# Optimization experiments

Measured on AMD Instinct MI355X. Metric: run time of the kernel, lower is better.

Reference implementation:

```python
import jax, jax.numpy as jnp
import numpy as np

B, S, D, H, L, V, DFF = 8, 1024, 256, 8, 4, 100, 1024
EPS = 1e-5


def _pos_encodings(seq_len, d):
    # Faithful to SinusoidalPositionalEmbedding (NOTE: original uses sin for both halves)
    pos = jnp.arange(seq_len, dtype=jnp.float32)[:, None]        # [S,1]
    freqs = jnp.arange(d, dtype=jnp.float32)[None, :]            # [1,D]
    sin_even = jnp.sin(pos / 10000.0 ** (freqs[:, 0::2] / d))    # [S,D/2]
    sin_odd = jnp.sin(pos / 10000.0 ** (freqs[:, 1::2] / d))     # [S,D/2]
    return jnp.concatenate([sin_even, sin_odd], axis=1)          # [S,D]


def _self_attention_mask(sequence_length, seq_len):
    # create_self_attention_mask with causal=True; assumes max(sequence_length)==seq_len
    r = jnp.arange(seq_len)[None, :]                             # [1,S]
    m = (r < sequence_length[:, None]).astype(jnp.float32)       # [B,S]
    m = m[:, :, None] * m[:, None, :]                            # [B,S,S]
    causal = jnp.tril(jnp.ones((seq_len, seq_len), jnp.float32))
    return m * causal                                            # [B,S,S]


def setup_inputs() -> dict:
    key = jax.random.key(0)
    ks = jax.random.split(key, 20)
    n = lambda k, shape, s=0.02: (jax.random.normal(k, shape) * s).astype(jnp.float32)
    return {
        "output_ids": jax.random.randint(ks[0], (B, S), 0, V),
        "target_sequence_length": jnp.full((B,), S, dtype=jnp.int32),
        "embedding": n(ks[1], (V, D), 1.0),
        "Wq": n(ks[2], (L, D, D)), "bq": jnp.zeros((L, D), jnp.float32),
        "Wk": n(ks[3], (L, D, D)), "bk": jnp.zeros((L, D), jnp.float32),
        "Wv": n(ks[4], (L, D, D)), "bv": jnp.zeros((L, D), jnp.float32),
        "Wo": n(ks[5], (L, D, D)), "bo": jnp.zeros((L, D), jnp.float32),
        "W1": n(ks[6], (L, D, DFF)), "b1": jnp.zeros((L, DFF), jnp.float32),
        "W2": n(ks[7], (L, DFF, D)), "b2": jnp.zeros((L, D), jnp.float32),
        "g1": jnp.ones((L, D), jnp.float32), "be1": jnp.zeros((L, D), jnp.float32),
        "g2": jnp.ones((L, D), jnp.float32), "be2": jnp.zeros((L, D), jnp.float32),
        "Wc": n(ks[8], (D, V)), "bc": jnp.zeros((V,), jnp.float32),
    }


def _forward(output_ids, target_sequence_length, embedding, Wq, bq, Wk, bk, Wv, bv,
             Wo, bo, W1, b1, W2, b2, g1, be1, g2, be2, Wc, bc):
    Bn, Sn = output_ids.shape
    d = embedding.shape[1]
    x = embedding[output_ids] + _pos_encodings(Sn, d)[None]      # [B,S,D]
    mask = _self_attention_mask(target_sequence_length, Sn)[:, None] > 0  # [B,1,S,S] bool

    def ln(h, g, b):
        m = h.mean(-1, keepdims=True)
        v = jnp.var(h, axis=-1, keepdims=True)
        return (h - m) / jnp.sqrt(v + EPS) * g + b

    def step(x, p):
        wq, bq_, wk, bk_, wv, bv_, wo, bo_, w1, b1_, w2, b2_, g1_, be1_, g2_, be2_ = p
        q = (x @ wq + bq_).reshape(Bn, Sn, H, -1)
        k = (x @ wk + bk_).reshape(Bn, Sn, H, -1)
        v = (x @ wv + bv_).reshape(Bn, Sn, H, -1)
        dh = q.shape[-1]
        scores = jnp.einsum('bqhd,bkhd->bhqk', q, k) / jnp.sqrt(jnp.float32(dh))
        attn = jax.nn.softmax(jnp.where(mask, scores, -1e9), axis=-1)
        attn = jnp.where(mask, attn, 0.0)                        # post-softmax mask (as original)
        y = jnp.einsum('bhqk,bkhd->bqhd', attn, v).reshape(Bn, Sn, -1)
        y = y @ wo + bo_
        x = ln(x + y, g1_, be1_)
        ff = jax.nn.relu(x @ w1 + b1_) @ w2 + b2_
        x = ln(x + ff, g2_, be2_)
        return x, None

    x, _ = jax.lax.scan(step, x, (Wq, bq, Wk, bk, Wv, bv, Wo, bo, W1, b1, W2, b2, g1, be1, g2, be2))
    return x @ Wc + bc                                           # logits [B,S,V]


def reference(output_ids, target_sequence_length, embedding, Wq, bq, Wk, bk, Wv, bv,
              Wo, bo, W1, b1, W2, b2, g1, be1, g2, be2, Wc, bc):
    return _forward(output_ids, target_sequence_length, embedding, Wq, bq, Wk, bk, Wv, bv,
                    Wo, bo, W1, b1, W2, b2, g1, be1, g2, be2, Wc, bc)
```

## Files before the change

### kernel.cpp

```cpp
#include <hip/hip_runtime.h>
#include <hip/hip_bf16.h>
#include <stdint.h>

#define B_   8
#define S_   1024
#define D_   256
#define H_   8
#define DH_  32
#define L_   4
#define V_   100
#define DFF_ 1024
#define M_   (B_*S_)

using bf16 = __hip_bfloat16;
typedef __bf16 bf16x8 __attribute__((ext_vector_type(8)));
typedef float  f32x4  __attribute__((ext_vector_type(4)));

static __device__ __forceinline__ float b2f(unsigned short u) {
  union { unsigned int i; float f; } w; w.i = ((unsigned int)u) << 16; return w.f;
}
static __device__ __forceinline__ unsigned short f2b(float f) {
  bf16 h = (bf16)f; return *(unsigned short*)&h;
}

static __device__ __forceinline__ void load_lds16(const void* g, void* l) {
  __builtin_amdgcn_global_load_lds((const __attribute__((address_space(1))) void*)g,
                                   (__attribute__((address_space(3))) void*)l,
                                   16, 0, 0);
}

#define SRC_CHS(tid)  ((((tid) & 3) ^ (((tid) >> 3) & 3)) * 8)
#define FRAG_Q8(quad, l15)  (((quad) ^ (((l15) >> 1) & 3)) * 8)

template<int CTRL>
static __device__ __forceinline__ float dppf(float v) {
  union { float f; int i; } a, r;
  a.f = v;
  r.i = __builtin_amdgcn_update_dpp(0, a.i, CTRL, 0xF, 0xF, true);
  return r.f;
}
static __device__ __forceinline__ float red_sum16(float v) {
  v += dppf<0xB1>(v);
  v += dppf<0x4E>(v);
  v += dppf<0x141>(v);
  v += dppf<0x140>(v);
  return v;
}

__global__ void prep_t(const float* __restrict__ Wq, const float* __restrict__ Wk,
                       const float* __restrict__ Wv, const float* __restrict__ Wo,
                       const float* __restrict__ W1, const float* __restrict__ W2,
                       const float* __restrict__ Wc,
                       const float* __restrict__ bq, const float* __restrict__ bk,
                       const float* __restrict__ bv,
                       bf16* __restrict__ WqkvT, bf16* __restrict__ WoT,
                       bf16* __restrict__ W1T, bf16* __restrict__ W2T,
                       bf16* __restrict__ WcT, float* __restrict__ bqkv)
{
  const int z = blockIdx.z;
  if (z == 25) {
    if (blockIdx.x || blockIdx.y) return;
    const int tid = threadIdx.y*32 + threadIdx.x;
    for (int i = tid; i < L_*768; i += 256) {
      const int l2 = i / 768, j = i % 768;
      const float* src = (j < 256) ? bq : (j < 512) ? bk : bv;
      bqkv[i] = src[l2*256 + (j & 255)];
    }
    return;
  }
  const float* src; bf16* dst; int R, C, Cd;
  if (z < 12) {
    const int l = z / 3, w = z % 3;
    src = ((w == 0) ? Wq : (w == 1) ? Wk : Wv) + (size_t)l*65536;
    R = 256; C = 256; Cd = 256;
    dst = WqkvT + (size_t)l*196608 + (size_t)w*65536;
  } else if (z < 16) {
    const int l = z - 12;
    src = Wo + (size_t)l*65536; R = 256; C = 256; Cd = 256;
    dst = WoT + (size_t)l*65536;
  } else if (z < 20) {
    const int l = z - 16;
    src = W1 + (size_t)l*262144; R = 256; C = 1024; Cd = 1024;
    dst = W1T + (size_t)l*262144;
  } else if (z < 24) {
    const int l = z - 20;
    src = W2 + (size_t)l*262144; R = 1024; C = 256; Cd = 256;
    dst = W2T + (size_t)l*262144;
  } else {
    src = Wc; R = 256; C = 100; Cd = 128;
    dst = WcT;
  }
  const int c0 = blockIdx.x*32, r0 = blockIdx.y*32;
  if (c0 >= Cd || r0 >= R) return;
  __shared__ float t[32][33];
  #pragma unroll
  for (int i = 0; i < 4; ++i) {
    const int r = r0 + threadIdx.y + i*8;
    const int c = c0 + threadIdx.x;
    t[threadIdx.y + i*8][threadIdx.x] = (r < R && c < C) ? src[(size_t)r*C + c] : 0.f;
  }
  __syncthreads();
  #pragma unroll
  for (int i = 0; i < 4; ++i) {
    const int c = c0 + threadIdx.y + i*8;
    const int r = r0 + threadIdx.x;
    if (c < Cd && r < R)
      dst[(size_t)c*R + r] = (bf16)t[threadIdx.x][threadIdx.y + i*8];
  }
}

__global__ void embed_kernel(const int* __restrict__ ids, const float* __restrict__ emb,
                             bf16* __restrict__ x)
{
  const int bs = blockIdx.x;
  const int d  = threadIdx.x;
  const int s  = bs & (S_-1);
  const int id = ids[bs];
  const int f  = (d < 128) ? (2*d) : (2*(d-128)+1);
  const float inv = powf(10000.f, -(float)f * (1.f/256.f));
  const float pe  = sinf((float)s * inv);
  x[(size_t)bs*D_ + d] = (bf16)(emb[(size_t)id*D_ + d] + pe);
}

__global__ __launch_bounds__(256) void gemm_qkv(
    const bf16* __restrict__ A, const bf16* __restrict__ BT,
    const float* __restrict__ bias,
    bf16* __restrict__ qp, bf16* __restrict__ kp, bf16* __restrict__ vt)
{
  __shared__ bf16 As[128*32];
  __shared__ bf16 Bs[64*32];
  __shared__ bf16 Vs[64][136];
  const int tid  = threadIdx.x;
  const int lane = tid & 63, wave = tid >> 6;
  const int quad = lane >> 4, l15 = lane & 15;
  const int m0 = blockIdx.x * 128;
  const int n0 = blockIdx.y * 64;
  const int wm = (wave & 1) * 64;
  const int wn = (wave >> 1) * 32;
  const int K = 256;

  const bf16* a0 = A  + (size_t)m0 * K;
  const bf16* b0 = BT + (size_t)n0 * K;
  const int row = tid >> 2;
  const int chs = SRC_CHS(tid);
  const int q8  = FRAG_Q8(quad, l15);

  f32x4 acc[4][2] = {};

  for (int k0 = 0; k0 < K; k0 += 32) {
    __syncthreads();
    load_lds16(a0 + (size_t)row*K      + k0 + chs, (char*)As + (size_t)wave*1024);
    load_lds16(a0 + (size_t)(row+64)*K + k0 + chs, (char*)As + 4096 + (size_t)wave*1024);
    load_lds16(b0 + (size_t)row*K      + k0 + chs, (char*)Bs + (size_t)wave*1024);
    __syncthreads();
    bf16x8 af[4], bfr[2];
    #pragma unroll
    for (int mt = 0; mt < 4; ++mt)
      af[mt] = *(const bf16x8*)(As + (wm + mt*16 + l15)*32 + q8);
    #pragma unroll
    for (int nt = 0; nt < 2; ++nt)
      bfr[nt] = *(const bf16x8*)(Bs + (wn + nt*16 + l15)*32 + q8);
    #pragma unroll
    for (int mt = 0; mt < 4; ++mt)
      #pragma unroll
      for (int nt = 0; nt < 2; ++nt)
        acc[mt][nt] = __builtin_amdgcn_mfma_f32_16x16x32_bf16(af[mt], bfr[nt], acc[mt][nt], 0, 0, 0);
  }

  const int seg = n0 >> 8;
  const int b  = m0 >> 10;
  const int s0 = m0 & 1023;

  if (seg < 2) {
    bf16* dst = seg ? kp : qp;
    const float sc = seg ? 1.f : (0.17677669529663687f * 1.4426950408889634f);
    #pragma unroll
    for (int nt = 0; nt < 2; ++nt) {
      const int n  = n0 + wn + nt*16 + l15;
      const int nn = n & 255;
      const int h = nn >> 5, d = nn & 31;
      const float bvs = bias[n];
      bf16* hb = dst + (((size_t)b*H_ + h)*S_)*DH_ + d;
      #pragma unroll
      for (int mt = 0; mt < 4; ++mt) {
        const int ml = wm + mt*16 + quad*4;
        #pragma unroll
        for (int r = 0; r < 4; ++r)
          hb[(size_t)(s0 + ml + r)*DH_] = (bf16)((acc[mt][nt][r] + bvs) * sc);
      }
    }
  } else {
    #pragma unroll
    for (int nt = 0; nt < 2; ++nt) {
      const int nl = wn + nt*16 + l15;
      const float bvs = bias[n0 + nl];
      #pragma unroll
      for (int mt = 0; mt < 4; ++mt) {
        const int ml = wm + mt*16 + quad*4;
        #pragma unroll
        for (int r = 0; r < 4; ++r)
          Vs[nl][ml + r] = (bf16)(acc[mt][nt][r] + bvs);
      }
    }
    __syncthreads();
    #pragma unroll
    for (int t = 0; t < 2; ++t) {
      const int vrow = (tid >> 3) + 32*t;
      const int soff = (tid & 7) * 16;
      const int nn = (n0 + vrow) & 255;
      const int h = nn >> 5, d = nn & 31;
      bf16* dst = vt + (((size_t)b*H_ + h)*DH_ + d)*S_ + s0 + soff;
      *(bf16x8*)dst       = *(const bf16x8*)&Vs[vrow][soff];
      *(bf16x8*)(dst + 8) = *(const bf16x8*)&Vs[vrow][soff + 8];
    }
  }
}

template<bool RELU, bool OUT_BF16>
__global__ __launch_bounds__(256) void gemm_bt(
    const bf16* __restrict__ A, const bf16* __restrict__ BT,
    const float* __restrict__ bias, void* __restrict__ C,
    int M, int N, int K)
{
  __shared__ bf16 As[128*32];
  __shared__ bf16 Bs[64*32];
  const int tid  = threadIdx.x;
  const int lane = tid & 63, wave = tid >> 6;
  const int quad = lane >> 4, l15 = lane & 15;
  const int m0 = blockIdx.x * 128;
  const int n0 = blockIdx.y * 64;
  const int wm = (wave & 1) * 64;
  const int wn = (wave >> 1) * 32;

  const bf16* a0 = A  + (size_t)m0 * K;
  const bf16* b0 = BT + (size_t)n0 * K;
  const int row = tid >> 2;
  const int chs = SRC_CHS(tid);
  const int q8  = FRAG_Q8(quad, l15);

  f32x4 acc[4][2] = {};

  for (int k0 = 0; k0 < K; k0 += 32) {
    __syncthreads();
    load_lds16(a0 + (size_t)row*K      + k0 + chs, (char*)As + (size_t)wave*1024);
    load_lds16(a0 + (size_t)(row+64)*K + k0 + chs, (char*)As + 4096 + (size_t)wave*1024);
    load_lds16(b0 + (size_t)row*K      + k0 + chs, (char*)Bs + (size_t)wave*1024);
    __syncthreads();
    bf16x8 af[4], bfr[2];
    #pragma unroll
    for (int mt = 0; mt < 4; ++mt)
      af[mt] = *(const bf16x8*)(As + (wm + mt*16 + l15)*32 + q8);
    #pragma unroll
    for (int nt = 0; nt < 2; ++nt)
      bfr[nt] = *(const bf16x8*)(Bs + (wn + nt*16 + l15)*32 + q8);
    #pragma unroll
    for (int mt = 0; mt < 4; ++mt)
      #pragma unroll
      for (int nt = 0; nt < 2; ++nt)
        acc[mt][nt] = __builtin_amdgcn_mfma_f32_16x16x32_bf16(af[mt], bfr[nt], acc[mt][nt], 0, 0, 0);
  }

  #pragma unroll
  for (int nt = 0; nt < 2; ++nt) {
    const int n = n0 + wn + nt*16 + l15;
    const float bvs = bias[n];
    #pragma unroll
    for (int mt = 0; mt < 4; ++mt) {
      const int mr = m0 + wm + mt*16 + quad*4;
      #pragma unroll
      for (int r = 0; r < 4; ++r) {
        float v = acc[mt][nt][r] + bvs;
        if (RELU) v = fmaxf(v, 0.f);
        if (OUT_BF16) ((bf16*)C)[(size_t)(mr + r)*N + n] = (bf16)v;
        else          ((float*)C)[(size_t)(mr + r)*N + n] = v;
      }
    }
  }
}

template<bool RELU, bool OUT_BF16, bool NMASK>
__global__ __launch_bounds__(256) void gemm_bt64(
    const bf16* __restrict__ A, const bf16* __restrict__ BT,
    const float* __restrict__ bias, void* __restrict__ C,
    int M, int N, int K)
{
  __shared__ bf16 As[64*32];
  __shared__ bf16 Bs[64*32];
  const int tid  = threadIdx.x;
  const int lane = tid & 63, wave = tid >> 6;
  const int quad = lane >> 4, l15 = lane & 15;
  const int m0 = blockIdx.x * 64;
  const int n0 = blockIdx.y * 64;
  const int wm = (wave & 1) * 32;
  const int wn = (wave >> 1) * 32;

  const bf16* a0 = A  + (size_t)m0 * K;
  const bf16* b0 = BT + (size_t)n0 * K;
  const int row = tid >> 2;
  const int chs = SRC_CHS(tid);
  const int q8  = FRAG_Q8(quad, l15);

  f32x4 acc[2][2] = {};

  for (int k0 = 0; k0 < K; k0 += 32) {
    __syncthreads();
    load_lds16(a0 + (size_t)row*K + k0 + chs, (char*)As + (size_t)wave*1024);
    load_lds16(b0 + (size_t)row*K + k0 + chs, (char*)Bs + (size_t)wave*1024);
    __syncthreads();
    bf16x8 af[2], bfr[2];
    #pragma unroll
    for (int mt = 0; mt < 2; ++mt)
      af[mt] = *(const bf16x8*)(As + (wm + mt*16 + l15)*32 + q8);
    #pragma unroll
    for (int nt = 0; nt < 2; ++nt)
      bfr[nt] = *(const bf16x8*)(Bs + (wn + nt*16 + l15)*32 + q8);
    #pragma unroll
    for (int mt = 0; mt < 2; ++mt)
      #pragma unroll
      for (int nt = 0; nt < 2; ++nt)
        acc[mt][nt] = __builtin_amdgcn_mfma_f32_16x16x32_bf16(af[mt], bfr[nt], acc[mt][nt], 0, 0, 0);
  }

  #pragma unroll
  for (int nt = 0; nt < 2; ++nt) {
    const int n = n0 + wn + nt*16 + l15;
    if (NMASK && n >= N) continue;
    const float bvs = bias[n];
    #pragma unroll
    for (int mt = 0; mt < 2; ++mt) {
      const int mr = m0 + wm + mt*16 + quad*4;
      #pragma unroll
      for (int r = 0; r < 4; ++r) {
        float v = acc[mt][nt][r] + bvs;
        if (RELU) v = fmaxf(v, 0.f);
        if (OUT_BF16) ((bf16*)C)[(size_t)(mr + r)*N + n] = (bf16)v;
        else          ((float*)C)[(size_t)(mr + r)*N + n] = v;
      }
    }
  }
}

__global__ __launch_bounds__(256) void gemm_ln(
    const bf16* __restrict__ A, const bf16* __restrict__ BT,
    const float* __restrict__ bias, const float* __restrict__ g,
    const float* __restrict__ be, bf16* xio, int K)
{
  __shared__ bf16 As[16*32];
  __shared__ bf16 Bs[256*32];
  __shared__ bf16 Xs[16][264];
  __shared__ float sums[4][16][2];

  const int tid  = threadIdx.x;
  const int lane = tid & 63, wave = tid >> 6;
  const int quad = lane >> 4, l15 = lane & 15;
  const int m0 = blockIdx.x * 16;
  const int wn = wave * 64;

  const bf16* a0 = A + (size_t)m0 * K;
  const int chs = SRC_CHS(tid);
  const int q8  = FRAG_Q8(quad, l15);

  f32x4 acc[4] = {};

  for (int k0 = 0; k0 < K; k0 += 32) {
    __syncthreads();
    if (wave == 0)
      load_lds16(a0 + (size_t)(lane >> 2)*K + k0 + SRC_CHS(lane), (char*)As);
    #pragma unroll
    for (int j = 0; j < 4; ++j)
      load_lds16(BT + (size_t)(64*j + (tid >> 2))*K + k0 + chs,
                 (char*)Bs + j*4096 + (size_t)wave*1024);
    __syncthreads();
    const bf16x8 af = *(const bf16x8*)(As + l15*32 + q8);
    #pragma unroll
    for (int nt = 0; nt < 4; ++nt) {
      const bf16x8 bfr = *(const bf16x8*)(Bs + (wn + nt*16 + l15)*32 + q8);
      acc[nt] = __builtin_amdgcn_mfma_f32_16x16x32_bf16(af, bfr, acc[nt], 0, 0, 0);
    }
  }

  {
    const int xr = tid >> 4, xc = (tid & 15) * 16;
    const bf16* src = xio + (size_t)(m0 + xr)*D_ + xc;
    *(bf16x8*)&Xs[xr][xc]     = *(const bf16x8*)src;
    *(bf16x8*)&Xs[xr][xc + 8] = *(const bf16x8*)(src + 8);
  }
  __syncthreads();

  float v[4][4];
  float bvs[4];
  #pragma unroll
  for (int nt = 0; nt < 4; ++nt) bvs[nt] = bias[wn + nt*16 + l15];
  #pragma unroll
  for (int r = 0; r < 4; ++r) {
    const int rr = quad*4 + r;
    float ls = 0.f, lq = 0.f;
    #pragma unroll
    for (int nt = 0; nt < 4; ++nt) {
      const float y = acc[nt][r] + bvs[nt];
      const float xv = b2f(*(const unsigned short*)&Xs[rr][wn + nt*16 + l15]);
      const float vv = xv + y;
      v[r][nt] = vv;
      ls += vv;
      lq += vv*vv;
    }
    ls = red_sum16(ls);
    lq = red_sum16(lq);
    if (l15 == 0) { sums[wave][rr][0] = ls; sums[wave][rr][1] = lq; }
  }
  __syncthreads();

  float gv[4], bev[4];
  #pragma unroll
  for (int nt = 0; nt < 4; ++nt) {
    gv[nt]  = g[wn + nt*16 + l15];
    bev[nt] = be[wn + nt*16 + l15];
  }
  #pragma unroll
  for (int r = 0; r < 4; ++r) {
    const int rr = quad*4 + r;
    const float ts = sums[0][rr][0] + sums[1][rr][0] + sums[2][rr][0] + sums[3][rr][0];
    const float tq = sums[0][rr][1] + sums[1][rr][1] + sums[2][rr][1] + sums[3][rr][1];
    const float mean = ts * (1.f/256.f);
    const float var  = tq * (1.f/256.f) - mean*mean;
    const float inv  = rsqrtf(var + 1e-5f);
    #pragma unroll
    for (int nt = 0; nt < 4; ++nt) {
      const bf16 o = (bf16)((v[r][nt] - mean)*inv*gv[nt] + bev[nt]);
      Xs[rr][wn + nt*16 + l15] = o;
    }
  }
  __syncthreads();

  {
    const int xr = tid >> 4, xc = (tid & 15) * 16;
    bf16* dst = xio + (size_t)(m0 + xr)*D_ + xc;
    *(bf16x8*)dst       = *(const bf16x8*)&Xs[xr][xc];
    *(bf16x8*)(dst + 8) = *(const bf16x8*)&Xs[xr][xc + 8];
  }
}

#define PSTR 68
__global__ __launch_bounds__(256) void attn_kernel(
    const bf16* __restrict__ qp, const bf16* __restrict__ kp,
    const bf16* __restrict__ vt, const int* __restrict__ tsl,
    bf16* __restrict__ out)
{
  const int h = blockIdx.y, b = blockIdx.z;
  const int lane = threadIdx.x & 63, wave = threadIdx.x >> 6;
  const int quad = lane >> 4, l15 = lane & 15;
  const int sid = blockIdx.x + wave*16;
  const int q0 = sid*16;
  const int len = tsl[b];

  __shared__ bf16 Pl[4][16*PSTR];

  const size_t bh = (size_t)b*H_ + h;
  const bf16* qb = qp + bh*S_*DH_;
  const bf16* kb = kp + bh*S_*DH_;
  const bf16* vb = vt + bh*DH_*S_;

  const bf16x8 qf = *(const bf16x8*)(qb + (size_t)(q0 + l15)*DH_ + quad*8);

  float lacc = 0.f;
  f32x4 o0 = {0.f,0.f,0.f,0.f}, o1 = {0.f,0.f,0.f,0.f};

  bf16* pw = &Pl[wave][0];
  const int qr = q0 + l15;
  const bool full = (len >= S_);
  const int dt = sid >> 2;

  bf16x8 kf[4];
  #pragma unroll
  for (int nt = 0; nt < 4; ++nt)
    kf[nt] = *(const bf16x8*)(kb + (size_t)(nt*16 + l15)*DH_ + quad*8);

  for (int ks = 0; ks <= dt; ++ks) {
    const int k0 = ks*64;
    bf16x8 vf[4];
    #pragma unroll
    for (int kc = 0; kc < 2; ++kc) {
      vf[kc*2]   = *(const bf16x8*)(vb + (size_t)l15*S_      + k0 + kc*32 + quad*8);
      vf[kc*2+1] = *(const bf16x8*)(vb + (size_t)(16+l15)*S_ + k0 + kc*32 + quad*8);
    }
    f32x4 s[4];
    #pragma unroll
    for (int nt = 0; nt < 4; ++nt) {
      const f32x4 z = {0.f,0.f,0.f,0.f};
      s[nt] = __builtin_amdgcn_mfma_f32_16x16x32_bf16(kf[nt], qf, z, 0, 0, 0);
    }
    bf16x8 kn[4];
    if (ks < dt) {
      const int k1 = k0 + 64;
      #pragma unroll
      for (int nt = 0; nt < 4; ++nt)
        kn[nt] = *(const bf16x8*)(kb + (size_t)(k1 + nt*16 + l15)*DH_ + quad*8);
    }
    #pragma unroll
    for (int nt = 0; nt < 4; ++nt) {
      float p0, p1, p2, p3;
      if (full && ks < dt) {
        p0 = exp2f(s[nt][0]);
        p1 = exp2f(s[nt][1]);
        p2 = exp2f(s[nt][2]);
        p3 = exp2f(s[nt][3]);
      } else {
        const int kbase = k0 + nt*16 + quad*4;
        const bool okq = (qr < len);
        p0 = (okq && kbase+0 <= qr && kbase+0 < len) ? exp2f(s[nt][0]) : 0.f;
        p1 = (okq && kbase+1 <= qr && kbase+1 < len) ? exp2f(s[nt][1]) : 0.f;
        p2 = (okq && kbase+2 <= qr && kbase+2 < len) ? exp2f(s[nt][2]) : 0.f;
        p3 = (okq && kbase+3 <= qr && kbase+3 < len) ? exp2f(s[nt][3]) : 0.f;
      }
      lacc += (p0 + p1) + (p2 + p3);
      uint2 w;
      w.x = (unsigned)f2b(p0) | ((unsigned)f2b(p1) << 16);
      w.y = (unsigned)f2b(p2) | ((unsigned)f2b(p3) << 16);
      *(uint2*)((char*)pw + l15*(PSTR*2) + nt*32 + quad*8) = w;
    }
    asm volatile("s_waitcnt lgkmcnt(0)" ::: "memory");
    #pragma unroll
    for (int kc = 0; kc < 2; ++kc) {
      const bf16x8 pf = *(const bf16x8*)(pw + l15*PSTR + kc*32 + quad*8);
      o0 = __builtin_amdgcn_mfma_f32_16x16x32_bf16(pf, vf[kc*2],   o0, 0, 0, 0);
      o1 = __builtin_amdgcn_mfma_f32_16x16x32_bf16(pf, vf[kc*2+1], o1, 0, 0, 0);
    }
    if (ks < dt) {
      #pragma unroll
      for (int nt = 0; nt < 4; ++nt) kf[nt] = kn[nt];
    }
  }

  float lt = lacc;
  lt += __shfl_xor(lt, 16);
  lt += __shfl_xor(lt, 32);

  bf16* ob = out + (size_t)b*S_*D_ + h*DH_;
  #pragma unroll
  for (int r = 0; r < 4; ++r) {
    const float lr = __shfl(lt, (lane & 48) | (quad*4 + r));
    const float inv = 1.f / fmaxf(lr, 1e-30f);
    const size_t rowoff = (size_t)(q0 + quad*4 + r)*D_;
    ob[rowoff + l15]      = (bf16)(o0[r]*inv);
    ob[rowoff + 16 + l15] = (bf16)(o1[r]*inv);
  }
}

extern "C" void kernel_launch(void* const* d_in, const int* in_sizes, int n_in,
                              void* d_out, int out_size, void* d_ws, size_t ws_size,
                              hipStream_t stream)
{
  const int*   ids = (const int*)d_in[0];
  const int*   tsl = (const int*)d_in[1];
  const float* emb = (const float*)d_in[2];
  const float* Wq  = (const float*)d_in[3];
  const float* bq  = (const float*)d_in[4];
  const float* Wk  = (const float*)d_in[5];
  const float* bk  = (const float*)d_in[6];
  const float* Wv  = (const float*)d_in[7];
  const float* bv  = (const float*)d_in[8];
  const float* Wo  = (const float*)d_in[9];
  const float* bo  = (const float*)d_in[10];
  const float* W1  = (const float*)d_in[11];
  const float* b1  = (const float*)d_in[12];
  const float* W2  = (const float*)d_in[13];
  const float* b2  = (const float*)d_in[14];
  const float* g1  = (const float*)d_in[15];
  const float* be1 = (const float*)d_in[16];
  const float* g2  = (const float*)d_in[17];
  const float* be2 = (const float*)d_in[18];
  const float* Wc  = (const float*)d_in[19];
  const float* bc  = (const float*)d_in[20];

  if (ws_size < (size_t)40*1024*1024) return;

  char* p = (char*)d_ws;
  auto carve = [&](size_t bytes) { void* r = (void*)p; p += (bytes + 255) & ~(size_t)255; return r; };
  bf16*  x     = (bf16*) carve((size_t)M_*D_*2);
  char*  big   = (char*) carve((size_t)M_*DFF_*2);
  char*  pkbuf = (char*) carve((size_t)12*1024*1024);
  bf16*  WqkvT = (bf16*) carve((size_t)L_*768*256*2);
  bf16*  WoT   = (bf16*) carve((size_t)L_*65536*2);
  bf16*  W1T   = (bf16*) carve((size_t)L_*262144*2);
  bf16*  W2T   = (bf16*) carve((size_t)L_*262144*2);
  bf16*  WcT   = (bf16*) carve((size_t)128*256*2);
  float* bqkv  = (float*)carve((size_t)L_*768*4);

  bf16*  aout = (bf16*)big;
  bf16*  ff1  = (bf16*)big;
  bf16*  qp   = (bf16*)pkbuf;
  bf16*  kp   = (bf16*)(pkbuf + (size_t)4*1024*1024);
  bf16*  vt   = (bf16*)(pkbuf + (size_t)8*1024*1024);

  prep_t<<<dim3(32,32,26), dim3(32,8), 0, stream>>>(Wq,Wk,Wv,Wo,W1,W2,Wc,bq,bk,bv,
                                                    WqkvT,WoT,W1T,W2T,WcT,bqkv);
  embed_kernel<<<dim3(M_), 256, 0, stream>>>(ids, emb, x);

  for (int l = 0; l < L_; ++l) {
    gemm_qkv<<<dim3(64,12), 256, 0, stream>>>(
        x, WqkvT + (size_t)l*768*256, bqkv + l*768, qp, kp, vt);
    attn_kernel<<<dim3(16,8,8), 256, 0, stream>>>(qp, kp, vt, tsl, aout);
    gemm_ln<<<dim3(512), 256, 0, stream>>>(
        aout, WoT + (size_t)l*65536, bo + l*256, g1 + l*256, be1 + l*256, x, 256);
    gemm_bt<true,true><<<dim3(64,16), 256, 0, stream>>>(
        x, W1T + (size_t)l*262144, b1 + l*1024, ff1, M_, 1024, 256);
    gemm_ln<<<dim3(512), 256, 0, stream>>>(
        ff1, W2T + (size_t)l*262144, b2 + l*256, g2 + l*256, be2 + l*256, x, 1024);
  }

  gemm_bt64<false,false,true><<<dim3(128,2), 256, 0, stream>>>(
      x, WcT, bc, (float*)d_out, M_, V_, 256);
}
```

Measured before the change: 464.1 us.

## Split attention key range across two blocks and combine partials

Each query tile's causal key range is split into two halves handled by separate blocks, doubling grid size, and a new combine kernel sums the unnormalized partial outputs and row sums before normalizing. This targets low occupancy and the load imbalance of the causal triangle, where late tiles do far more work. It drops the K register prefetch in favour of direct loads, sets launch bounds for higher occupancy, and adds an extra kernel launch plus a round trip of partial results through global memory. Partial outputs are stored in bf16 before summation, which slightly changes rounding.

```diff
diff --git a/kernel.cpp b/kernel.cpp
--- a/kernel.cpp
+++ b/kernel.cpp
@@ -441,15 +441,16 @@
 }
 
 #define PSTR 68
-__global__ __launch_bounds__(256) void attn_kernel(
+__global__ __launch_bounds__(256, 8) void attn_kernel(
     const bf16* __restrict__ qp, const bf16* __restrict__ kp,
     const bf16* __restrict__ vt, const int* __restrict__ tsl,
-    bf16* __restrict__ out)
+    bf16* __restrict__ po, float* __restrict__ pl)
 {
   const int h = blockIdx.y, b = blockIdx.z;
   const int lane = threadIdx.x & 63, wave = threadIdx.x >> 6;
   const int quad = lane >> 4, l15 = lane & 15;
-  const int sid = blockIdx.x + wave*16;
+  const int c   = blockIdx.x >> 4;
+  const int sid = (blockIdx.x & 15) + wave*16;
   const int q0 = sid*16;
   const int len = tsl[b];
 
@@ -469,32 +470,25 @@
   const int qr = q0 + l15;
   const bool full = (len >= S_);
   const int dt = sid >> 2;
-
-  bf16x8 kf[4];
-  #pragma unroll
-  for (int nt = 0; nt < 4; ++nt)
-    kf[nt] = *(const bf16x8*)(kb + (size_t)(nt*16 + l15)*DH_ + quad*8);
-
-  for (int ks = 0; ks <= dt; ++ks) {
+  const int ntiles = dt + 1;
+  const int c0e = (ntiles + 1) >> 1;
+  const int ts = c ? c0e : 0;
+  const int te = c ? ntiles : c0e;
+
+  for (int ks = ts; ks < te; ++ks) {
     const int k0 = ks*64;
+    f32x4 s[4];
+    #pragma unroll
+    for (int nt = 0; nt < 4; ++nt) {
+      const bf16x8 kf = *(const bf16x8*)(kb + (size_t)(k0 + nt*16 + l15)*DH_ + quad*8);
+      const f32x4 z = {0.f,0.f,0.f,0.f};
+      s[nt] = __builtin_amdgcn_mfma_f32_16x16x32_bf16(kf, qf, z, 0, 0, 0);
+    }
     bf16x8 vf[4];
     #pragma unroll
     for (int kc = 0; kc < 2; ++kc) {
       vf[kc*2]   = *(const bf16x8*)(vb + (size_t)l15*S_      + k0 + kc*32 + quad*8);
       vf[kc*2+1] = *(const bf16x8*)(vb + (size_t)(16+l15)*S_ + k0 + kc*32 + quad*8);
-    }
-    f32x4 s[4];
-    #pragma unroll
-    for (int nt = 0; nt < 4; ++nt) {
-      const f32x4 z = {0.f,0.f,0.f,0.f};
-      s[nt] = __builtin_amdgcn_mfma_f32_16x16x32_bf16(kf[nt], qf, z, 0, 0, 0);
-    }
-    bf16x8 kn[4];
-    if (ks < dt) {
-      const int k1 = k0 + 64;
-      #pragma unroll
-      for (int nt = 0; nt < 4; ++nt)
-        kn[nt] = *(const bf16x8*)(kb + (size_t)(k1 + nt*16 + l15)*DH_ + quad*8);
     }
     #pragma unroll
     for (int nt = 0; nt < 4; ++nt) {
@@ -525,25 +519,44 @@
       o0 = __builtin_amdgcn_mfma_f32_16x16x32_bf16(pf, vf[kc*2],   o0, 0, 0, 0);
       o1 = __builtin_amdgcn_mfma_f32_16x16x32_bf16(pf, vf[kc*2+1], o1, 0, 0, 0);
     }
-    if (ks < dt) {
-      #pragma unroll
-      for (int nt = 0; nt < 4; ++nt) kf[nt] = kn[nt];
-    }
   }
 
   float lt = lacc;
   lt += __shfl_xor(lt, 16);
   lt += __shfl_xor(lt, 32);
 
-  bf16* ob = out + (size_t)b*S_*D_ + h*DH_;
+  bf16* pb = po + (((size_t)c*64 + bh)*S_ + q0)*DH_;
   #pragma unroll
   for (int r = 0; r < 4; ++r) {
-    const float lr = __shfl(lt, (lane & 48) | (quad*4 + r));
-    const float inv = 1.f / fmaxf(lr, 1e-30f);
-    const size_t rowoff = (size_t)(q0 + quad*4 + r)*D_;
-    ob[rowoff + l15]      = (bf16)(o0[r]*inv);
-    ob[rowoff + 16 + l15] = (bf16)(o1[r]*inv);
-  }
+    const int row = quad*4 + r;
+    pb[(size_t)row*DH_ + l15]      = (bf16)o0[r];
+    pb[(size_t)row*DH_ + 16 + l15] = (bf16)o1[r];
+  }
+  if (quad == 0)
+    pl[((size_t)c*64 + bh)*S_ + q0 + l15] = lt;
+}
+
+__global__ void attn_combine(const bf16* __restrict__ po, const float* __restrict__ pl,
+                             bf16* __restrict__ aout)
+{
+  const int t = blockIdx.x*256 + threadIdx.x;
+  const int dc  = t & 3;
+  const int row = (t >> 2) & 1023;
+  const int bh  = t >> 12;
+  const float l0 = pl[(size_t)bh*S_ + row];
+  const float l1 = pl[(size_t)(64 + bh)*S_ + row];
+  const float inv = 1.f / fmaxf(l0 + l1, 1e-30f);
+  const bf16* p0 = po + ((size_t)bh*S_ + row)*DH_ + dc*8;
+  const bf16* p1 = po + ((size_t)(64 + bh)*S_ + row)*DH_ + dc*8;
+  const bf16x8 a = *(const bf16x8*)p0;
+  const bf16x8 bb = *(const bf16x8*)p1;
+  const int b = bh >> 3, h = bh & 7;
+  bf16* dst = aout + ((size_t)b*S_ + row)*D_ + h*DH_ + dc*8;
+  bf16x8 o;
+  #pragma unroll
+  for (int i = 0; i < 8; ++i)
+    o[i] = (__bf16)(((float)a[i] + (float)bb[i]) * inv);
+  *(bf16x8*)dst = o;
 }
 
 extern "C" void kernel_launch(void* const* d_in, const int* in_sizes, int n_in,
@@ -586,8 +599,10 @@
   bf16*  WcT   = (bf16*) carve((size_t)128*256*2);
   float* bqkv  = (float*)carve((size_t)L_*768*4);
 
-  bf16*  aout = (bf16*)big;
-  bf16*  ff1  = (bf16*)big;
+  bf16*  aout = (bf16*) big;
+  bf16*  po   = (bf16*)(big + (size_t)4*1024*1024);
+  float* pl   = (float*)(big + (size_t)12*1024*1024);
+  bf16*  ff1  = (bf16*) big;
   bf16*  qp   = (bf16*)pkbuf;
   bf16*  kp   = (bf16*)(pkbuf + (size_t)4*1024*1024);
   bf16*  vt   = (bf16*)(pkbuf + (size_t)8*1024*1024);
@@ -599,7 +614,8 @@
   for (int l = 0; l < L_; ++l) {
     gemm_qkv<<<dim3(64,12), 256, 0, stream>>>(
         x, WqkvT + (size_t)l*768*256, bqkv + l*768, qp, kp, vt);
-    attn_kernel<<<dim3(16,8,8), 256, 0, stream>>>(qp, kp, vt, tsl, aout);
+    attn_kernel<<<dim3(32,8,8), 256, 0, stream>>>(qp, kp, vt, tsl, po, pl);
+    attn_combine<<<dim3(1024), 256, 0, stream>>>(po, pl, aout);
     gemm_ln<<<dim3(512), 256, 0, stream>>>(
         aout, WoT + (size_t)l*65536, bo + l*256, g1 + l*256, be1 + l*256, x, 256);
     gemm_bt<true,true><<<dim3(64,16), 256, 0, stream>>>(
```

Result: slower. 499.0 us (+7.5%).
